# Performance work log

Hardware: AMD Instinct MI355X
Metric: run time of the kernel (lower is better)

## Reference

```python
import jax, jax.numpy as jnp
import numpy as np

S, FEAT, D, H, L, DFF, C = 1024, 64, 512, 8, 2, 2048, 10
DB = D // 4  # distance-bias MLP hidden
NFREQ = D // 6  # 85 -> 6*85=510 dims, padded to 512
EPS = 1e-5


def _layernorm(x, g, b):
    mu = jnp.mean(x, axis=-1, keepdims=True)
    var = jnp.mean(jnp.square(x - mu), axis=-1, keepdims=True)
    return (x - mu) * jax.lax.rsqrt(var + EPS) * g + b


def setup_inputs() -> dict:
    key = jax.random.key(0)
    ks = iter(jax.random.split(key, 40))
    def w(shape, scale=0.02):
        return (jax.random.normal(next(ks), shape, jnp.float32) * scale)
    inp = {
        'features': jax.random.normal(next(ks), (S, FEAT), jnp.float32),
        'positions': jax.random.uniform(next(ks), (S, 3), jnp.float32),
        'freq_bands': jnp.asarray(10.0 ** np.linspace(0.0, 10.0, NFREQ), jnp.float32),
        'in_w': w((FEAT, D)), 'in_b': jnp.zeros((D,), jnp.float32),
        'qw': w((L, D, D)), 'qb': jnp.zeros((L, D), jnp.float32),
        'kw': w((L, D, D)), 'kb': jnp.zeros((L, D), jnp.float32),
        'vw': w((L, D, D)), 'vb': jnp.zeros((L, D), jnp.float32),
        'ow': w((L, D, D)), 'ob': jnp.zeros((L, D), jnp.float32),
        'db1w': w((L, 1, DB), 0.5), 'db1b': jnp.zeros((L, DB), jnp.float32),
        'db2w': w((L, DB, H), 0.1), 'db2b': jnp.zeros((L, H), jnp.float32),
        'n1g': jnp.ones((L, D), jnp.float32), 'n1b': jnp.zeros((L, D), jnp.float32),
        'n2g': jnp.ones((L, D), jnp.float32), 'n2b': jnp.zeros((L, D), jnp.float32),
        'f1w': w((L, D, DFF)), 'f1b': jnp.zeros((L, DFF), jnp.float32),
        'f2w': w((L, DFF, D)), 'f2b': jnp.zeros((L, D), jnp.float32),
        'c1w': w((D, D // 2)), 'c1b': jnp.zeros((D // 2,), jnp.float32),
        'c2w': w((D // 2, C)), 'c2b': jnp.zeros((C,), jnp.float32),
    }
    return inp


def _forward(features, positions, freq_bands, in_w, in_b, qw, qb, kw, kb, vw, vb,
             ow, ob, db1w, db1b, db2w, db2b, n1g, n1b, n2g, n2b,
             f1w, f1b, f2w, f2b, c1w, c1b, c2w, c2b):
    d_model = in_w.shape[1]
    nhead = db2w.shape[-1]
    head_dim = d_model // nhead
    scale = 1.0 / np.sqrt(head_dim)

    x = features[None] @ in_w + in_b            # [1, S, D]
    pos = positions[None]                        # [1, S, 3]

    # 3D sinusoidal positional encoding: [sin0,cos0,sin1,cos1,sin2,cos2]
    enc = []
    for i in range(3):
        cs = pos[..., i:i + 1] * freq_bands      # [1, S, NFREQ] (broadcast)
        enc.append(jnp.sin(cs))
        enc.append(jnp.cos(cs))
    pe = jnp.concatenate(enc, axis=-1)           # [1, S, 6*NFREQ]
    if pe.shape[-1] > d_model:
        pe = pe[..., :d_model]
    elif pe.shape[-1] < d_model:
        pe = jnp.pad(pe, ((0, 0), (0, 0), (0, d_model - pe.shape[-1])))
    x = x + pe

    # pairwise distances [1, S, S, 1]; safe sqrt (zero grad on diagonal)
    diff = pos[:, :, None, :] - pos[:, None, :, :]
    sq = jnp.sum(jnp.square(diff), axis=-1, keepdims=True)
    dist = jnp.sqrt(jnp.where(sq > 0, sq, 1.0)) * (sq > 0)

    n_layers = qw.shape[0]
    seq = x.shape[1]
    for l in range(n_layers):
        q = (x @ qw[l] + qb[l]).reshape(1, seq, nhead, head_dim)
        k = (x @ kw[l] + kb[l]).reshape(1, seq, nhead, head_dim)
        v = (x @ vw[l] + vb[l]).reshape(1, seq, nhead, head_dim)
        scores = jnp.einsum('bihd,bjhd->bhij', q, k) * scale  # [1,H,S,S]
        hbias = jax.nn.relu(dist @ db1w[l] + db1b[l])          # [1,S,S,DB]
        bias = jnp.einsum('bijc,ch->bhij', hbias, db2w[l]) + db2b[l][None, :, None, None]
        attn = jax.nn.softmax(scores + bias, axis=-1)
        out = jnp.einsum('bhij,bjhd->bihd', attn, v).reshape(1, seq, d_model)
        out = out @ ow[l] + ob[l]
        x = _layernorm(x + out, n1g[l], n1b[l])
        ffn = jax.nn.relu(x @ f1w[l] + f1b[l]) @ f2w[l] + f2b[l]
        x = _layernorm(x + ffn, n2g[l], n2b[l])

    pooled = jnp.mean(x, axis=1)                 # [1, D]
    return jax.nn.relu(pooled @ c1w + c1b) @ c2w + c2b  # [1, C]


def reference(features, positions, freq_bands, in_w, in_b, qw, qb, kw, kb, vw, vb,
              ow, ob, db1w, db1b, db2w, db2b, n1g, n1b, n2g, n2b,
              f1w, f1b, f2w, f2b, c1w, c1b, c2w, c2b):
    return _forward(features, positions, freq_bands, in_w, in_b, qw, qb, kw, kb, vw, vb,
                    ow, ob, db1w, db1b, db2w, db2b, n1g, n1b, n2g, n2b,
                    f1w, f1b, f2w, f2b, c1w, c1b, c2w, c2b)
```

## Files before the change

### kernel.cpp

```cpp
#include <hip/hip_runtime.h>

namespace {
constexpr int kS   = 1024;
constexpr int kD   = 512;
constexpr int kDFF = 2048;
constexpr int kNF  = 85;
}

typedef __attribute__((ext_vector_type(8))) short bhalf8_t;
typedef _Float16 half8_t __attribute__((ext_vector_type(8)));
typedef __attribute__((ext_vector_type(4))) float f32x4_t;

__device__ __forceinline__ float wave_sum(float v) {
#pragma unroll
    for (int o = 1; o < 64; o <<= 1) v += __shfl_xor(v, o, 64);
    return v;
}
__device__ __forceinline__ unsigned short f2h(float f) {
    _Float16 h = (_Float16)f;
    return __builtin_bit_cast(unsigned short, h);
}
__device__ __forceinline__ float h2f(unsigned short u) {
    return (float)__builtin_bit_cast(_Float16, u);
}

__device__ __forceinline__ void tr_tile32(const float* __restrict__ in,
                                          unsigned short* __restrict__ out,
                                          int N, int K, int k0, int n0, int t,
                                          float* tile )
{
    int r = t >> 3, c4 = (t & 7) * 4;
    float4 v = *reinterpret_cast<const float4*>(&in[(long)(k0 + r) * N + n0 + c4]);
    tile[r * 33 + c4] = v.x; tile[r * 33 + c4 + 1] = v.y;
    tile[r * 33 + c4 + 2] = v.z; tile[r * 33 + c4 + 3] = v.w;
    __syncthreads();
    int nr = t >> 3, kq = (t & 7) * 4;
    unsigned short h[4];
#pragma unroll
    for (int j = 0; j < 4; ++j) h[j] = f2h(tile[(kq + j) * 33 + nr]);
    *reinterpret_cast<ushort4*>(&out[(long)(n0 + nr) * K + k0 + kq]) =
        make_ushort4(h[0], h[1], h[2], h[3]);
}

__global__ __launch_bounds__(256)
void prep_k(const float* __restrict__ feat, const float* __restrict__ pos,
            const float* __restrict__ fb, const float* __restrict__ in_w,
            const float* __restrict__ in_b, float* __restrict__ x,
            unsigned short* __restrict__ xb, float* __restrict__ dist,
            const float* __restrict__ qw, const float* __restrict__ kw,
            const float* __restrict__ vw, const float* __restrict__ ow,
            unsigned short* __restrict__ qwb, unsigned short* __restrict__ kwb,
            unsigned short* __restrict__ vwb, unsigned short* __restrict__ owb,
            const float* __restrict__ f1w, unsigned short* __restrict__ f1wb,
            const float* __restrict__ f2w, unsigned short* __restrict__ f2wb,
            const float* __restrict__ a_, const float* __restrict__ b_,
            const float* __restrict__ w2, const float* __restrict__ b2,
            float* __restrict__ bp_out, float* __restrict__ Atab,
            float* __restrict__ Btab)
{
    __shared__ float smem[1056];
    int bid = blockIdx.x;
    int t = threadIdx.x;
    if (bid < 256) {
        int s0 = bid * 4;
        smem[t] = feat[s0 * 64 + t];
        __syncthreads();
        float b0 = in_b[t], b1 = in_b[t + 256];
        float a0[4] = {b0, b0, b0, b0}, a1[4] = {b1, b1, b1, b1};
#pragma unroll 4
        for (int c = 0; c < 64; ++c) {
            float w0 = in_w[c * kD + t], w1 = in_w[c * kD + 256 + t];
#pragma unroll
            for (int r = 0; r < 4; ++r) {
                a0[r] = fmaf(smem[r * 64 + c], w0, a0[r]);
                a1[r] = fmaf(smem[r * 64 + c], w1, a1[r]);
            }
        }
#pragma unroll
        for (int r = 0; r < 4; ++r) {
            int s = s0 + r;
            float pe0 = 0.f, pe1 = 0.f;
            int d = t;
            if (d < 6 * kNF) {
                int seg = d / kNF, idx = d - seg * kNF;
                float cs = pos[s * 3 + (seg >> 1)] * fb[idx];
                pe0 = (seg & 1) ? cosf(cs) : sinf(cs);
            }
            d = t + 256;
            if (d < 6 * kNF) {
                int seg = d / kNF, idx = d - seg * kNF;
                float cs = pos[s * 3 + (seg >> 1)] * fb[idx];
                pe1 = (seg & 1) ? cosf(cs) : sinf(cs);
            }
            float o0 = a0[r] + pe0, o1 = a1[r] + pe1;
            x[s * kD + t]        = o0;
            x[s * kD + 256 + t]  = o1;
            xb[s * kD + t]       = f2h(o0);
            xb[s * kD + 256 + t] = f2h(o1);
        }
    } else if (bid < 1280) {
        int i = bid - 256;
        float px = pos[i * 3], py = pos[i * 3 + 1], pz = pos[i * 3 + 2];
        for (int j = t; j < kS; j += 256) {
            float dx = px - pos[j * 3], dy = py - pos[j * 3 + 1], dz = pz - pos[j * 3 + 2];
            float sq = dx * dx + dy * dy + dz * dz;
            dist[(long)i * kS + j] = sq > 0.f ? sqrtf(sq) : 0.f;
        }
    } else if (bid < 7424) {
        int idx = bid - 1280;
        if (idx < 2048) {
            int zz = idx >> 8, rem = idx & 255;
            int mat = zz >> 1, layer = zz & 1;
            const float* in = (mat == 0) ? qw : (mat == 1) ? kw : (mat == 2) ? vw : ow;
            unsigned short* out = (mat == 0) ? qwb : (mat == 1) ? kwb : (mat == 2) ? vwb : owb;
            tr_tile32(in + (long)layer * 262144, out + (long)layer * 262144,
                      512, 512, (rem & 15) * 32, (rem >> 4) * 32, t, smem);
        } else if (idx < 4096) {
            int l = idx - 2048;
            int z = l >> 10;
            tr_tile32(f1w + (long)z * 1048576, f1wb + (long)z * 1048576,
                      2048, 512, (l & 15) * 32, ((l >> 4) & 63) * 32, t, smem);
        } else {
            int l = idx - 4096;
            int z = l >> 10;
            tr_tile32(f2w + (long)z * 1048576, f2wb + (long)z * 1048576,
                      512, 2048, (l & 63) * 32, ((l >> 6) & 15) * 32, t, smem);
        }
    } else {
        int l = bid - 7424;
        int seg = l % 129, ly = l / 129;
        const float* ap = a_ + ly * 128;
        const float* bpp = b_ + ly * 128;
        const float* w2p = w2 + ly * 1024;
        const float* b2p = b2 + ly * 8;
        float* At = Atab + ly * 1040;
        float* Bt = Btab + ly * 1040;

        if (t < 128) {
            float a = ap[t], b = bpp[t];
            smem[t] = (a != 0.f) ? (-b / a) : 3.0e38f;
        }
        __syncthreads();
        for (int ksz = 2; ksz <= 128; ksz <<= 1) {
            for (int j = ksz >> 1; j > 0; j >>= 1) {
                if (t < 128) {
                    int ixj = t ^ j;
                    if (ixj > t) {
                        bool up = ((t & ksz) == 0);
                        float x0 = smem[t], x1 = smem[ixj];
                        if ((x0 > x1) == up) { smem[t] = x1; smem[ixj] = x0; }
                    }
                }
                __syncthreads();
            }
        }
        float m;
        if (seg == 0)        m = smem[0] - 1.0f;
        else if (seg == 128) m = smem[127] + 1.0f;
        else                 m = 0.5f * (smem[seg - 1] + smem[seg]);
        if (seg == 0 && t < 128) bp_out[ly * 128 + t] = smem[t];
        __syncthreads();

        int h = t & 7, cg = t >> 3;
        float A = 0.f, B = 0.f;
#pragma unroll
        for (int j = 0; j < 4; ++j) {
            int c = cg * 4 + j;
            float a = ap[c], b = bpp[c];
            if (fmaf(a, m, b) > 0.f) {
                float w = w2p[c * 8 + h];
                A = fmaf(a, w, A);
                B = fmaf(b, w, B);
            }
        }
#pragma unroll
        for (int off = 8; off < 64; off <<= 1) {
            A += __shfl_xor(A, off, 64);
            B += __shfl_xor(B, off, 64);
        }
        int w = t >> 6, lane = t & 63;
        if (lane < 8) { smem[w * 8 + lane] = A; smem[32 + w * 8 + lane] = B; }
        __syncthreads();
        if (t < 8) {
            float At_ = smem[t] + smem[8 + t] + smem[16 + t] + smem[24 + t];
            float Bt_ = smem[32 + t] + smem[40 + t] + smem[48 + t] + smem[56 + t];
            At[seg * 8 + t] = At_;
            Bt[seg * 8 + t] = Bt_ + b2p[t];
        }
    }
}

constexpr int BKp = 72;
constexpr int ASZ = 64 * BKp;
constexpr int BSZ = 128 * BKp;

template<int K>
__device__ __forceinline__ void gemm_core(
    const unsigned short* __restrict__ Ap, const unsigned short* __restrict__ Bp,
    int lda, int ldb, int bm, int bn, int tid,
    unsigned short* __restrict__ As, unsigned short* __restrict__ Bs,
    f32x4_t acc[2][4])
{
    int w = tid >> 6, lane = tid & 63, quad = lane >> 4, l16 = lane & 15;
    int wm = (w >> 1) * 32, wn = (w & 1) * 64;
    int ar = tid >> 2, ac = (tid & 3) * 16;
    int br = tid >> 1, bc = (tid & 1) * 32;
    const unsigned short* pa = Ap + (long)(bm + ar) * lda + ac;
    const unsigned short* pb = Bp + (long)(bn + br) * ldb + bc;

    bhalf8_t a0_0, a0_1, b0_0, b0_1, b0_2, b0_3;
    bhalf8_t a1_0, a1_1, b1_0, b1_1, b1_2, b1_3;

#define LDG(S, k0) do { \
    a##S##_0 = *reinterpret_cast<const bhalf8_t*>(pa + (k0)); \
    a##S##_1 = *reinterpret_cast<const bhalf8_t*>(pa + (k0) + 8); \
    b##S##_0 = *reinterpret_cast<const bhalf8_t*>(pb + (k0)); \
    b##S##_1 = *reinterpret_cast<const bhalf8_t*>(pb + (k0) + 8); \
    b##S##_2 = *reinterpret_cast<const bhalf8_t*>(pb + (k0) + 16); \
    b##S##_3 = *reinterpret_cast<const bhalf8_t*>(pb + (k0) + 24); } while (0)
#define STG(S, as, bs) do { \
    *reinterpret_cast<bhalf8_t*>(&(as)[ar * BKp + ac])      = a##S##_0; \
    *reinterpret_cast<bhalf8_t*>(&(as)[ar * BKp + ac + 8])  = a##S##_1; \
    *reinterpret_cast<bhalf8_t*>(&(bs)[br * BKp + bc])      = b##S##_0; \
    *reinterpret_cast<bhalf8_t*>(&(bs)[br * BKp + bc + 8])  = b##S##_1; \
    *reinterpret_cast<bhalf8_t*>(&(bs)[br * BKp + bc + 16]) = b##S##_2; \
    *reinterpret_cast<bhalf8_t*>(&(bs)[br * BKp + bc + 24]) = b##S##_3; } while (0)

    constexpr int NT = K / 64;
    LDG(0, 0);
    STG(0, As, Bs);
    if (NT > 1) LDG(1, 64);
#pragma unroll
    for (int t = 0; t < NT; ++t) {
        __syncthreads();
        if (t + 2 < NT) {
            if ((t & 1) == 0) LDG(0, (t + 2) * 64);
            else              LDG(1, (t + 2) * 64);
        }
        const unsigned short* as = As + (t & 1) * ASZ;
        const unsigned short* bs = Bs + (t & 1) * BSZ;
#pragma unroll
        for (int kq = 0; kq < 2; ++kq) {
            bhalf8_t af[2], bf[4];
#pragma unroll
            for (int i = 0; i < 2; ++i)
                af[i] = *reinterpret_cast<const bhalf8_t*>(
                    &as[(wm + i * 16 + l16) * BKp + kq * 32 + quad * 8]);
#pragma unroll
            for (int j = 0; j < 4; ++j)
                bf[j] = *reinterpret_cast<const bhalf8_t*>(
                    &bs[(wn + j * 16 + l16) * BKp + kq * 32 + quad * 8]);
#pragma unroll
            for (int i = 0; i < 2; ++i)
#pragma unroll
                for (int j = 0; j < 4; ++j)
                    acc[i][j] = __builtin_amdgcn_mfma_f32_16x16x32_f16(
                        __builtin_bit_cast(half8_t, af[i]), __builtin_bit_cast(half8_t, bf[j]),
                        acc[i][j], 0, 0, 0);
        }
        if (t + 1 < NT) {
            if (((t + 1) & 1) == 0) STG(0, As, Bs);
            else                    STG(1, As + ASZ, Bs + BSZ);
        }
    }
#undef LDG
#undef STG
}

__global__ __launch_bounds__(256, 2)
void qkv_bias_k(const unsigned short* __restrict__ xb,
                const unsigned short* __restrict__ qwb, const unsigned short* __restrict__ kwb,
                const unsigned short* __restrict__ vwb,
                const float* __restrict__ qbias, const float* __restrict__ kbias,
                const float* __restrict__ vbias,
                unsigned short* __restrict__ qb2, unsigned short* __restrict__ kb2,
                unsigned short* __restrict__ vtb,
                const float* __restrict__ dist, const float* __restrict__ bp,
                const float* __restrict__ Atab, const float* __restrict__ Btab,
                unsigned short* __restrict__ bmap, unsigned int* __restrict__ cnt)
{
    __shared__ __align__(16) unsigned short smem[2 * ASZ + 2 * BSZ];
    int bid = blockIdx.x;
    int tid = threadIdx.x;
    if (bid < 192) {
        int z = bid >> 6, rem = bid & 63;
        int bm = (rem & 15) * 64, bn = (rem >> 4) * 128;
        const unsigned short* Bp = (z == 1) ? kwb : (z == 2) ? vwb : qwb;
        const float* bias = (z == 1) ? kbias : (z == 2) ? vbias : qbias;
        f32x4_t acc[2][4] = {};
        gemm_core<512>(xb, Bp, 512, 512, bm, bn, tid, smem, smem + 2 * ASZ, acc);

        int w = tid >> 6, lane = tid & 63, quad = lane >> 4, l16 = lane & 15;
        int wm = (w >> 1) * 32, wn = (w & 1) * 64;
        if (z == 2) {
            __syncthreads();
            unsigned short* T = smem;
#pragma unroll
            for (int j = 0; j < 4; ++j) {
                int ln = wn + j * 16 + l16;
                float bv = bias[bn + ln];
#pragma unroll
                for (int i = 0; i < 2; ++i)
#pragma unroll
                    for (int r = 0; r < 4; ++r)
                        T[ln * BKp + wm + i * 16 + quad * 4 + r] =
                            f2h((acc[i][j][r] + bv) * 1024.f);
            }
            __syncthreads();
            int nr = tid >> 1, mc = (tid & 1) * 32;
            int gn = bn + nr;
            unsigned short* dst = vtb + (long)(gn >> 6) * 65536
                                + (long)(gn & 63) * 1024 + bm + mc;
#pragma unroll
            for (int jj = 0; jj < 4; ++jj)
                *reinterpret_cast<bhalf8_t*>(dst + jj * 8) =
                    *reinterpret_cast<const bhalf8_t*>(&T[nr * BKp + mc + jj * 8]);
        } else {
#pragma unroll
            for (int j = 0; j < 4; ++j) {
                int n = bn + wn + j * 16 + l16;
                float bv = bias[n];
                unsigned short* dst = ((z == 1) ? kb2 : qb2)
                    + (long)(n >> 6) * 131072 + (n & 63);
#pragma unroll
                for (int i = 0; i < 2; ++i)
#pragma unroll
                    for (int r = 0; r < 4; ++r) {
                        int m = bm + wm + i * 16 + quad * 4 + r;
                        float s = acc[i][j][r] + bv;
                        unsigned short hi = f2h(s);
                        dst[(long)m * 128]      = hi;
                        dst[(long)m * 128 + 64] = (z == 0) ? f2h(s - h2f(hi)) : hi;
                    }
            }
        }
    } else {
        if (bid == 192 && tid < 8) cnt[tid] = 0;
        float* fs = reinterpret_cast<float*>(smem);
        float* bps = fs;
        float* Ah  = fs + 128;
        float* Bh  = fs + 1160;
        int t = tid;
        if (t < 128) bps[t] = bp[t];
        for (int i = t; i < 1032; i += 256) { Ah[i] = Atab[i]; Bh[i] = Btab[i]; }
        __syncthreads();
        long i = ((long)(bid - 192) * 256 + t) * 4;
        float4 d4 = *reinterpret_cast<const float4*>(dist + i);
        float dv[4] = {d4.x, d4.y, d4.z, d4.w};
        int seg[4];
#pragma unroll
        for (int j = 0; j < 4; ++j) {
            float tv = dv[j];
            int lo = 0, hi = 128;
            while (lo < hi) { int mid = (lo + hi) >> 1; if (bps[mid] < tv) lo = mid + 1; else hi = mid; }
            seg[j] = lo;
        }
        long gm  = i >> 10;
        int gn0  = (int)(i & 1023);
        int zz   = gn0 >> 7, nb = (gn0 >> 4) & 7, c4 = gn0 & 15;
        long pbase = gm * 1024 + zz * 128 + nb;
#pragma unroll
        for (int h = 0; h < 8; ++h) {
            unsigned short* bh = bmap + (long)h * 1048576 + pbase;
#pragma unroll
            for (int j = 0; j < 4; ++j)
                bh[(c4 + j) * 8] =
                    f2h(fmaf(Ah[seg[j] * 8 + h], dv[j], Bh[seg[j] * 8 + h]));
        }
    }
}

__global__ __launch_bounds__(256, 2)
void bgemm_ffn1_k(const unsigned short* __restrict__ A,
                  const unsigned short* __restrict__ B,
                  const float* __restrict__ bias,
                  unsigned short* __restrict__ hb)
{
    __shared__ __align__(16) unsigned short smem[2 * ASZ + 2 * BSZ];
    int tid = threadIdx.x;
    int bm = blockIdx.x * 64, bn = blockIdx.y * 128;
    f32x4_t acc[2][4] = {};
    gemm_core<512>(A, B, 512, 512, bm, bn, tid, smem, smem + 2 * ASZ, acc);

    int w = tid >> 6, lane = tid & 63, quad = lane >> 4, l16 = lane & 15;
    int wm = (w >> 1) * 32, wn = (w & 1) * 64;
#pragma unroll
    for (int j = 0; j < 4; ++j) {
        int n = bn + wn + j * 16 + l16;
        float bv = bias[n];
#pragma unroll
        for (int i = 0; i < 2; ++i)
#pragma unroll
            for (int r = 0; r < 4; ++r) {
                int m = bm + wm + i * 16 + quad * 4 + r;
                hb[(long)m * kDFF + n] = f2h(fmaxf(acc[i][j][r] + bv, 0.f));
            }
    }
}

template<int K>
__global__ __launch_bounds__(256, 2)
void bgemm_k(const unsigned short* __restrict__ A, const unsigned short* __restrict__ B,
             int N, int lda, int ldb, unsigned short* __restrict__ Cpart)
{
    __shared__ __align__(16) unsigned short smem[2 * ASZ + 2 * BSZ];
    int tid = threadIdx.x;
    int ks = blockIdx.z;
    const unsigned short* Ap = A + (long)ks * K;
    const unsigned short* Bp = B + (long)ks * K;
    int bm = blockIdx.x * 64, bn = blockIdx.y * 128;
    f32x4_t acc[2][4] = {};
    gemm_core<K>(Ap, Bp, lda, ldb, bm, bn, tid, smem, smem + 2 * ASZ, acc);

    int w = tid >> 6, lane = tid & 63, quad = lane >> 4, l16 = lane & 15;
    int wm = (w >> 1) * 32, wn = (w & 1) * 64;
    unsigned short* Cp = Cpart + (long)ks * kS * N;
#pragma unroll
    for (int i = 0; i < 2; ++i)
#pragma unroll
        for (int j = 0; j < 4; ++j)
#pragma unroll
            for (int r = 0; r < 4; ++r) {
                int m = bm + wm + i * 16 + quad * 4 + r;
                int n = bn + wn + j * 16 + l16;
                Cp[(long)m * N + n] = f2h(acc[i][j][r]);
            }
}

__global__ __launch_bounds__(256, 2)
void bgemm_oproj_k(const unsigned short* __restrict__ po,
                   const float* __restrict__ pm, const float* __restrict__ pl,
                   const unsigned short* __restrict__ Bw,
                   unsigned short* __restrict__ Cpart)
{
    __shared__ __align__(16) unsigned short As[2 * ASZ];
    __shared__ __align__(16) unsigned short Bs[2 * BSZ];
    __shared__ float wz_s[2][64][9];
    __shared__ float inv_s[2][64];

    int tid = threadIdx.x;
    int ks = blockIdx.z;
    int bm = blockIdx.x * 64, bn = blockIdx.y * 128;
    int h0 = ks * 2;

    int br = tid >> 1, bc = (tid & 1) * 32;
    {
        const unsigned short* pb = Bw + (long)(bn + br) * 512 + ks * 128 + bc;
#pragma unroll
        for (int t = 0; t < 2; ++t) {
            bhalf8_t v0 = *reinterpret_cast<const bhalf8_t*>(pb + t * 64);
            bhalf8_t v1 = *reinterpret_cast<const bhalf8_t*>(pb + t * 64 + 8);
            bhalf8_t v2 = *reinterpret_cast<const bhalf8_t*>(pb + t * 64 + 16);
            bhalf8_t v3 = *reinterpret_cast<const bhalf8_t*>(pb + t * 64 + 24);
            unsigned short* bs = Bs + t * BSZ;
            *reinterpret_cast<bhalf8_t*>(&bs[br * BKp + bc])      = v0;
            *reinterpret_cast<bhalf8_t*>(&bs[br * BKp + bc + 8])  = v1;
            *reinterpret_cast<bhalf8_t*>(&bs[br * BKp + bc + 16]) = v2;
            *reinterpret_cast<bhalf8_t*>(&bs[br * BKp + bc + 24]) = v3;
        }
    }

    if (tid < 128) {
        int t = tid >> 6, r = tid & 63;
        long sidx = (long)(h0 + t) * 1024 + bm + r;
        float m[8], M = -3.0e38f;
#pragma unroll
        for (int z = 0; z < 8; ++z) { m[z] = pm[z * 8192 + sidx]; M = fmaxf(M, m[z]); }
        float lt = 0.f;
#pragma unroll
        for (int z = 0; z < 8; ++z) {
            float w = __expf(m[z] - M);
            wz_s[t][r][z] = w;
            lt = fmaf(pl[z * 8192 + sidx], w, lt);
        }
        inv_s[t][r] = 1.f / lt;
    }
    __syncthreads();

    int ar = tid >> 2, ac = (tid & 3) * 16;
#pragma unroll
    for (int t = 0; t < 2; ++t) {
        float inv = inv_s[t][ar];
        const unsigned short* p = po + ((long)(h0 + t) * 1024 + bm + ar) * 64 + ac;
        float acc[16] = {};
#pragma unroll
        for (int z = 0; z < 8; ++z) {
            float w = wz_s[t][ar][z];
            bhalf8_t v0 = *reinterpret_cast<const bhalf8_t*>(p + (long)z * 524288);
            bhalf8_t v1 = *reinterpret_cast<const bhalf8_t*>(p + (long)z * 524288 + 8);
#pragma unroll
            for (int j = 0; j < 8; ++j) {
                acc[j]     = fmaf(h2f((unsigned short)v0[j]), w, acc[j]);
                acc[8 + j] = fmaf(h2f((unsigned short)v1[j]), w, acc[8 + j]);
            }
        }
        unsigned short* as = As + t * ASZ;
#pragma unroll
        for (int j = 0; j < 16; ++j)
            as[ar * BKp + ac + j] = f2h(acc[j] * inv);
    }
    __syncthreads();

    int w = tid >> 6, lane = tid & 63, quad = lane >> 4, l16 = lane & 15;
    int wm = (w >> 1) * 32, wn = (w & 1) * 64;
    f32x4_t accf[2][4] = {};
#pragma unroll
    for (int t = 0; t < 2; ++t) {
        const unsigned short* as = As + t * ASZ;
        const unsigned short* bs = Bs + t * BSZ;
#pragma unroll
        for (int kq = 0; kq < 2; ++kq) {
            bhalf8_t af[2], bf[4];
#pragma unroll
            for (int i = 0; i < 2; ++i)
                af[i] = *reinterpret_cast<const bhalf8_t*>(
                    &as[(wm + i * 16 + l16) * BKp + kq * 32 + quad * 8]);
#pragma unroll
            for (int j = 0; j < 4; ++j)
                bf[j] = *reinterpret_cast<const bhalf8_t*>(
                    &bs[(wn + j * 16 + l16) * BKp + kq * 32 + quad * 8]);
#pragma unroll
            for (int i = 0; i < 2; ++i)
#pragma unroll
                for (int j = 0; j < 4; ++j)
                    accf[i][j] = __builtin_amdgcn_mfma_f32_16x16x32_f16(
                        __builtin_bit_cast(half8_t, af[i]), __builtin_bit_cast(half8_t, bf[j]),
                        accf[i][j], 0, 0, 0);
        }
    }

    unsigned short* Cp = Cpart + (long)ks * kS * 512;
#pragma unroll
    for (int i = 0; i < 2; ++i)
#pragma unroll
        for (int j = 0; j < 4; ++j)
#pragma unroll
            for (int r = 0; r < 4; ++r) {
                int m = bm + wm + i * 16 + quad * 4 + r;
                int n = bn + wn + j * 16 + l16;
                Cp[(long)m * 512 + n] = f2h(accf[i][j][r]);
            }
}

__global__ __launch_bounds__(256, 3)
void flash_part_k(const unsigned short* __restrict__ qb2, const unsigned short* __restrict__ kb2,
                  const unsigned short* __restrict__ vtb, const unsigned short* __restrict__ bmap,
                  unsigned short* __restrict__ po, float* __restrict__ pm, float* __restrict__ pl)
{
    constexpr int KP = 136;
    __shared__ __align__(16) unsigned short Klds[128 * KP];
    __shared__ __align__(16) unsigned short Vlds[64 * KP];

    int tid = threadIdx.x;
    int w    = tid >> 6;
    int lane = tid & 63;
    int quad = lane >> 4, l16 = lane & 15;

    int wg  = blockIdx.x;
    int lin = (wg & 7) * 128 + (wg >> 3);
    int qbg = lin & 15;
    int h   = (lin >> 4) & 7;
    int z   = lin >> 7;
    int qb  = qbg * 4 + w;
    int bm  = qb * 16;
    int k0  = z * 128;

    const unsigned short* Qh = qb2 + (long)h * 131072;
    const unsigned short* Kh = kb2 + (long)h * 131072;
    const unsigned short* Vh = vtb + (long)h * 65536;
    const unsigned short* Bm = bmap + (long)h * 1048576;

    {
        int kr = tid >> 1, kc = (tid & 1) * 64;
#pragma unroll
        for (int j = 0; j < 8; ++j)
            *reinterpret_cast<bhalf8_t*>(&Klds[kr * KP + kc + j * 8]) =
                *reinterpret_cast<const bhalf8_t*>(&Kh[(long)(k0 + kr) * 128 + kc + j * 8]);
        int vr = tid >> 2, vc = (tid & 3) * 32;
#pragma unroll
        for (int j = 0; j < 4; ++j)
            *reinterpret_cast<bhalf8_t*>(&Vlds[vr * KP + vc + j * 8]) =
                *reinterpret_cast<const bhalf8_t*>(&Vh[(long)vr * 1024 + k0 + vc + j * 8]);
    }

    bhalf8_t aq[4];
#pragma unroll
    for (int kq = 0; kq < 4; ++kq)
        aq[kq] = *reinterpret_cast<const bhalf8_t*>(
            &Qh[(long)(bm + l16) * 128 + kq * 32 + quad * 8]);
    bhalf8_t bias8[4];
#pragma unroll
    for (int r = 0; r < 4; ++r) {
        int gm = bm + quad * 4 + r;
        bias8[r] = *reinterpret_cast<const bhalf8_t*>(
            &Bm[(long)gm * 1024 + z * 128 + l16 * 8]);
    }

    __syncthreads();

    f32x4_t sacc[8] = {};
#pragma unroll
    for (int kq = 0; kq < 4; ++kq) {
        bhalf8_t bk[8];
#pragma unroll
        for (int nb = 0; nb < 8; ++nb)
            bk[nb] = *reinterpret_cast<const bhalf8_t*>(
                &Klds[(nb * 16 + l16) * KP + kq * 32 + quad * 8]);
#pragma unroll
        for (int nb = 0; nb < 8; ++nb)
            sacc[nb] = __builtin_amdgcn_mfma_f32_16x16x32_f16(
                __builtin_bit_cast(half8_t, aq[kq]), __builtin_bit_cast(half8_t, bk[nb]),
                sacc[nb], 0, 0, 0);
    }

    float m_r[4] = {-3.0e38f, -3.0e38f, -3.0e38f, -3.0e38f};
#pragma unroll
    for (int nb = 0; nb < 8; ++nb)
#pragma unroll
        for (int r = 0; r < 4; ++r) {
            float bias = h2f((unsigned short)bias8[r][nb]);
            float s = fmaf(sacc[nb][r], 0.125f, bias);
            sacc[nb][r] = s;
            m_r[r] = fmaxf(m_r[r], s);
        }
#pragma unroll
    for (int r = 0; r < 4; ++r) {
        float m_ = m_r[r];
#pragma unroll
        for (int off = 1; off < 16; off <<= 1) m_ = fmaxf(m_, __shfl_xor(m_, off, 64));
        m_r[r] = m_;
    }

    __syncthreads();

    unsigned short* Ps = Klds + w * 16 * KP;
    float l_r[4];
#pragma unroll
    for (int r = 0; r < 4; ++r) {
        int row = quad * 4 + r;
        float mN = m_r[r];
        float s_ = 0.f;
#pragma unroll
        for (int nb = 0; nb < 8; ++nb) {
            float p = __expf(sacc[nb][r] - mN);
            Ps[row * KP + nb * 16 + l16] = f2h(p * 16384.f);
            s_ += p;
        }
#pragma unroll
        for (int off = 1; off < 16; off <<= 1) s_ += __shfl_xor(s_, off, 64);
        l_r[r] = s_;
    }

    long sbase = (((long)z * 8 + h) * 64 + qb) * 16;
    if (l16 == 0) {
#pragma unroll
        for (int r = 0; r < 4; ++r) {
            pm[sbase + quad * 4 + r] = m_r[r];
            pl[sbase + quad * 4 + r] = l_r[r];
        }
    }

    f32x4_t oacc[4] = {};
#pragma unroll
    for (int kq2 = 0; kq2 < 4; ++kq2) {
        bhalf8_t ap = *reinterpret_cast<const bhalf8_t*>(&Ps[l16 * KP + kq2 * 32 + quad * 8]);
#pragma unroll
        for (int j2 = 0; j2 < 4; ++j2) {
            bhalf8_t bv = *reinterpret_cast<const bhalf8_t*>(
                &Vlds[(j2 * 16 + l16) * KP + kq2 * 32 + quad * 8]);
            oacc[j2] = __builtin_amdgcn_mfma_f32_16x16x32_f16(
                __builtin_bit_cast(half8_t, ap), __builtin_bit_cast(half8_t, bv),
                oacc[j2], 0, 0, 0);
        }
    }

    unsigned short* pob = po + sbase * 64;
#pragma unroll
    for (int j2 = 0; j2 < 4; ++j2)
#pragma unroll
        for (int r = 0; r < 4; ++r)
            pob[(quad * 4 + r) * 64 + j2 * 16 + l16] =
                f2h(oacc[j2][r] * (1.f / 16777216.f));
}

__global__ __launch_bounds__(256)
void add_ln_fused_k(const unsigned short* __restrict__ part, float* __restrict__ x,
                    const float* __restrict__ bias,
                    const float* __restrict__ g, const float* __restrict__ b,
                    unsigned short* __restrict__ xb, int splitk)
{
    __shared__ float sm[4];
    int row = blockIdx.x, t = threadIdx.x;
    const long MN = (long)kS * kD;
    float* xr = x + (long)row * kD;
    float s0 = 0.f, s1 = 0.f;
    const unsigned short* pr = part + (long)row * kD;
    for (int sl = 0; sl < splitk; ++sl) {
        s0 += h2f(pr[(long)sl * MN + t]);
        s1 += h2f(pr[(long)sl * MN + t + 256]);
    }
    s0 += bias[t] + xr[t];
    s1 += bias[t + 256] + xr[t + 256];
    float sum = wave_sum(s0 + s1);
    if ((t & 63) == 0) sm[t >> 6] = sum;
    __syncthreads();
    sum = sm[0] + sm[1] + sm[2] + sm[3];
    float mu = sum * (1.f / kD);
    float d0 = s0 - mu, d1 = s1 - mu;
    __syncthreads();
    float vs = wave_sum(d0 * d0 + d1 * d1);
    if ((t & 63) == 0) sm[t >> 6] = vs;
    __syncthreads();
    vs = sm[0] + sm[1] + sm[2] + sm[3];
    float rs = rsqrtf(vs * (1.f / kD) + 1e-5f);
    float o0 = fmaf(d0 * rs, g[t], b[t]);
    float o1 = fmaf(d1 * rs, g[t + 256], b[t + 256]);
    xr[t]       = o0;
    xr[t + 256] = o1;
    unsigned short* xrow = xb + (long)row * 512;
    xrow[t]       = f2h(o0);
    xrow[t + 256] = f2h(o1);
}

__global__ __launch_bounds__(256)
void pool_head_k(const float* __restrict__ x, float* __restrict__ partial,
                 float* __restrict__ h1g, unsigned int* __restrict__ cnt2,
                 const float* __restrict__ c1w, const float* __restrict__ c1b,
                 const float* __restrict__ c2w, const float* __restrict__ c2b,
                 float* __restrict__ out)
{
    __shared__ float pooled[kD];
    __shared__ int flag;
    int t = threadIdx.x;
    int bid = blockIdx.x;
    int cb = bid & 1, rb = bid >> 1;
    int col = cb * 256 + t;
    float s = 0.f;
    for (int r = rb * 128; r < rb * 128 + 128; ++r) s += x[(long)r * kD + col];
    partial[rb * kD + col] = s;

    __threadfence();
    if (t == 0) {
        atomicAdd(&cnt2[0], 1u);
        while (atomicAdd(&cnt2[0], 0u) < 16u) {}
    }
    __syncthreads();
    __threadfence();

    {
        float p0 = 0.f, p1 = 0.f;
#pragma unroll
        for (int r = 0; r < 8; ++r) {
            p0 += partial[r * kD + t];
            p1 += partial[r * kD + t + 256];
        }
        pooled[t]       = p0 * (1.0f / kS);
        pooled[t + 256] = p1 * (1.0f / kS);
    }
    __syncthreads();

    {
        int c = bid * 16 + (t >> 4);
        int sub = t & 15;
        float a = 0.f;
        for (int f = sub; f < kD; f += 16)
            a = fmaf(pooled[f], c1w[(long)f * 256 + c], a);
#pragma unroll
        for (int o = 1; o < 16; o <<= 1) a += __shfl_xor(a, o, 64);
        if (sub == 0) h1g[c] = fmaxf(a + c1b[c], 0.f);
    }

    __threadfence();
    if (t == 0) flag = (atomicAdd(&cnt2[1], 1u) == 15u);
    __syncthreads();
    if (!flag) return;
    __threadfence();

    if (t < 160) {
        int c = t >> 4, sub = t & 15;
        float a = 0.f;
        for (int f = sub; f < 256; f += 16)
            a = fmaf(h1g[f], c2w[(long)f * 10 + c], a);
#pragma unroll
        for (int o = 1; o < 16; o <<= 1) a += __shfl_xor(a, o, 64);
        if (sub == 0) out[c] = a + c2b[c];
    }
}

extern "C" void kernel_launch(void* const* d_in, const int* in_sizes, int n_in,
                              void* d_out, int out_size, void* d_ws, size_t ws_size,
                              hipStream_t stream)
{
    (void)in_sizes; (void)n_in; (void)out_size; (void)ws_size;
    const float* features = (const float*)d_in[0];
    const float* positions= (const float*)d_in[1];
    const float* fb       = (const float*)d_in[2];
    const float* in_w     = (const float*)d_in[3];
    const float* in_b     = (const float*)d_in[4];
    const float* qw  = (const float*)d_in[5];
    const float* qb  = (const float*)d_in[6];
    const float* kw  = (const float*)d_in[7];
    const float* kb  = (const float*)d_in[8];
    const float* vw  = (const float*)d_in[9];
    const float* vb  = (const float*)d_in[10];
    const float* ow  = (const float*)d_in[11];
    const float* ob  = (const float*)d_in[12];
    const float* db1w= (const float*)d_in[13];
    const float* db1b= (const float*)d_in[14];
    const float* db2w= (const float*)d_in[15];
    const float* db2b= (const float*)d_in[16];
    const float* n1g = (const float*)d_in[17];
    const float* n1b = (const float*)d_in[18];
    const float* n2g = (const float*)d_in[19];
    const float* n2b = (const float*)d_in[20];
    const float* f1w = (const float*)d_in[21];
    const float* f1b = (const float*)d_in[22];
    const float* f2w = (const float*)d_in[23];
    const float* f2b = (const float*)d_in[24];
    const float* c1w = (const float*)d_in[25];
    const float* c1b = (const float*)d_in[26];
    const float* c2w = (const float*)d_in[27];
    const float* c2b = (const float*)d_in[28];

    float* ws = (float*)d_ws;
    const long SD = (long)kS * kD;
    float* x      = ws;
    float* dist   = ws + 3 * SD;
    float* part_f = ws + 5 * SD;
    float* bpw    = ws + 17 * SD;
    float* Atab   = bpw + 256;
    float* Btab   = Atab + 2080;
    float* partial= Btab + 2080;

    unsigned short* part16 = (unsigned short*)part_f;
    unsigned short* po     = (unsigned short*)part_f;
    float* pmv = part_f + 2162688;
    float* plv = pmv + 65536;
    unsigned int* cnt2 = (unsigned int*)(plv + 65536);
    float* h1g = (float*)(cnt2 + 16);
    unsigned short* part16b = (unsigned short*)(part_f + 2294048);

    unsigned short* ub = (unsigned short*)(ws + 17 * SD + 8512);
    unsigned short* xb   = ub;
    unsigned short* qb2  = ub   + 1048576;
    unsigned short* kb2  = qb2  + 1048576;
    unsigned short* vtb  = kb2  + 1048576;
    unsigned short* hb   = vtb  + 524288;
    unsigned short* qwb  = hb   + 2097152;
    unsigned short* kwb  = qwb  + 524288;
    unsigned short* vwb  = kwb  + 524288;
    unsigned short* owb  = vwb  + 524288;
    unsigned short* f1wb = owb  + 524288;
    unsigned short* f2wb = f1wb + 2097152;
    unsigned short* bmap = f2wb + 2097152;

    prep_k<<<7682, 256, 0, stream>>>(features, positions, fb, in_w, in_b, x, xb,
                                     dist, qw, kw, vw, ow, qwb, kwb, vwb, owb,
                                     f1w, f1wb, f2w, f2wb,
                                     db1w, db1b, db2w, db2b, bpw, Atab, Btab);

    for (int l = 0; l < 2; ++l) {
        qkv_bias_k<<<1216, 256, 0, stream>>>(
            xb, qwb + l * 262144, kwb + l * 262144, vwb + l * 262144,
            qb + l * kD, kb + l * kD, vb + l * kD, qb2, kb2, vtb,
            dist, bpw + l * 128, Atab + l * 1040, Btab + l * 1040, bmap, cnt2);

        flash_part_k<<<1024, 256, 0, stream>>>(
            qb2, kb2, vtb, bmap, po, pmv, plv);

        bgemm_oproj_k<<<dim3(16, 4, 4), 256, 0, stream>>>(
            po, pmv, plv, owb + l * 262144, part16b);
        add_ln_fused_k<<<kS, 256, 0, stream>>>(
            part16b, x, ob + l * kD, n1g + l * kD, n1b + l * kD, xb, 4);

        bgemm_ffn1_k<<<dim3(16, 16), 256, 0, stream>>>(
            xb, f1wb + l * 1048576, f1b + l * kDFF, hb);

        bgemm_k<512><<<dim3(16, 4, 4), 256, 0, stream>>>(
            hb, f2wb + l * 1048576, 512, 2048, 2048, part16);
        add_ln_fused_k<<<kS, 256, 0, stream>>>(
            part16, x, f2b + l * kD, n2g + l * kD, n2b + l * kD, xb, 4);
    }

    pool_head_k<<<16, 256, 0, stream>>>(x, partial, h1g, cnt2,
                                        c1w, c1b, c2w, c2b, (float*)d_out);
}
```

Before: 283.5 us.

## Stage GEMM tiles with direct global-to-LDS loads and XOR-swizzled layout

Rewrites the shared GEMM core so tiles are copied straight from global memory into LDS with global_load_lds, instead of being loaded into registers and then stored to LDS. The padded 72-element row stride is replaced by an unpadded 64-wide layout with an XOR swizzle, to avoid LDS bank conflicts on the MFMA fragment reads. The prefetch depth drops from two register stages to a single LDS double buffer. This aims to save VGPRs and LDS store instructions, at the cost of depending on correct waitcnt handling for the asynchronous LDS writes before each barrier.

```diff
diff --git a/kernel.cpp b/kernel.cpp
--- a/kernel.cpp
+++ b/kernel.cpp
@@ -190,9 +190,18 @@
     }
 }
 
+constexpr int ASZ2 = 64 * 64;
+constexpr int BSZ2 = 128 * 64;
+
 constexpr int BKp = 72;
 constexpr int ASZ = 64 * BKp;
 constexpr int BSZ = 128 * BKp;
+
+__device__ __forceinline__ void gload16(const unsigned short* g, unsigned short* l) {
+    __builtin_amdgcn_global_load_lds(
+        (const __attribute__((address_space(1))) unsigned int*)g,
+        (__attribute__((address_space(3))) unsigned int*)l, 16, 0, 0);
+}
 
 template<int K>
 __device__ __forceinline__ void gemm_core(
@@ -203,53 +212,44 @@
 {
     int w = tid >> 6, lane = tid & 63, quad = lane >> 4, l16 = lane & 15;
     int wm = (w >> 1) * 32, wn = (w & 1) * 64;
-    int ar = tid >> 2, ac = (tid & 3) * 16;
-    int br = tid >> 1, bc = (tid & 1) * 32;
-    const unsigned short* pa = Ap + (long)(bm + ar) * lda + ac;
-    const unsigned short* pb = Bp + (long)(bn + br) * ldb + bc;
-
-    bhalf8_t a0_0, a0_1, b0_0, b0_1, b0_2, b0_3;
-    bhalf8_t a1_0, a1_1, b1_0, b1_1, b1_2, b1_3;
-
-#define LDG(S, k0) do { \
-    a##S##_0 = *reinterpret_cast<const bhalf8_t*>(pa + (k0)); \
-    a##S##_1 = *reinterpret_cast<const bhalf8_t*>(pa + (k0) + 8); \
-    b##S##_0 = *reinterpret_cast<const bhalf8_t*>(pb + (k0)); \
-    b##S##_1 = *reinterpret_cast<const bhalf8_t*>(pb + (k0) + 8); \
-    b##S##_2 = *reinterpret_cast<const bhalf8_t*>(pb + (k0) + 16); \
-    b##S##_3 = *reinterpret_cast<const bhalf8_t*>(pb + (k0) + 24); } while (0)
-#define STG(S, as, bs) do { \
-    *reinterpret_cast<bhalf8_t*>(&(as)[ar * BKp + ac])      = a##S##_0; \
-    *reinterpret_cast<bhalf8_t*>(&(as)[ar * BKp + ac + 8])  = a##S##_1; \
-    *reinterpret_cast<bhalf8_t*>(&(bs)[br * BKp + bc])      = b##S##_0; \
-    *reinterpret_cast<bhalf8_t*>(&(bs)[br * BKp + bc + 8])  = b##S##_1; \
-    *reinterpret_cast<bhalf8_t*>(&(bs)[br * BKp + bc + 16]) = b##S##_2; \
-    *reinterpret_cast<bhalf8_t*>(&(bs)[br * BKp + bc + 24]) = b##S##_3; } while (0)
+    int lr = lane >> 3;
+    int sw = (lane & 7) ^ lr;
+
+    const unsigned short* pa  = Ap + (long)(bm + w * 16 + lr) * lda + sw * 8;
+    const unsigned short* pa2 = pa + (long)8 * lda;
+    const unsigned short* pb  = Bp + (long)(bn + w * 32 + lr) * ldb + sw * 8;
+
+    auto stage = [&](int k0, int buf) {
+        unsigned short* as = As + buf * ASZ2 + w * 16 * 64;
+        unsigned short* bs = Bs + buf * BSZ2 + w * 32 * 64;
+        gload16(pa + k0, as);
+        gload16(pa2 + k0, as + 8 * 64);
+#pragma unroll
+        for (int j = 0; j < 4; ++j)
+            gload16(pb + (long)(j * 8) * ldb + k0, bs + j * 8 * 64);
+    };
 
     constexpr int NT = K / 64;
-    LDG(0, 0);
-    STG(0, As, Bs);
-    if (NT > 1) LDG(1, 64);
+    stage(0, 0);
+    int r7 = l16 & 7;
 #pragma unroll
     for (int t = 0; t < NT; ++t) {
         __syncthreads();
-        if (t + 2 < NT) {
-            if ((t & 1) == 0) LDG(0, (t + 2) * 64);
-            else              LDG(1, (t + 2) * 64);
-        }
-        const unsigned short* as = As + (t & 1) * ASZ;
-        const unsigned short* bs = Bs + (t & 1) * BSZ;
+        if (t + 1 < NT) stage((t + 1) * 64, (t + 1) & 1);
+        const unsigned short* as = As + (t & 1) * ASZ2;
+        const unsigned short* bs = Bs + (t & 1) * BSZ2;
 #pragma unroll
         for (int kq = 0; kq < 2; ++kq) {
+            int slot = ((kq * 4 + quad) ^ r7) * 8;
             bhalf8_t af[2], bf[4];
 #pragma unroll
             for (int i = 0; i < 2; ++i)
                 af[i] = *reinterpret_cast<const bhalf8_t*>(
-                    &as[(wm + i * 16 + l16) * BKp + kq * 32 + quad * 8]);
+                    &as[(wm + i * 16 + l16) * 64 + slot]);
 #pragma unroll
             for (int j = 0; j < 4; ++j)
                 bf[j] = *reinterpret_cast<const bhalf8_t*>(
-                    &bs[(wn + j * 16 + l16) * BKp + kq * 32 + quad * 8]);
+                    &bs[(wn + j * 16 + l16) * 64 + slot]);
 #pragma unroll
             for (int i = 0; i < 2; ++i)
 #pragma unroll
@@ -258,13 +258,7 @@
                         __builtin_bit_cast(half8_t, af[i]), __builtin_bit_cast(half8_t, bf[j]),
                         acc[i][j], 0, 0, 0);
         }
-        if (t + 1 < NT) {
-            if (((t + 1) & 1) == 0) STG(0, As, Bs);
-            else                    STG(1, As + ASZ, Bs + BSZ);
-        }
-    }
-#undef LDG
-#undef STG
+    }
 }
 
 __global__ __launch_bounds__(256, 2)
@@ -279,7 +273,7 @@
                 const float* __restrict__ Atab, const float* __restrict__ Btab,
                 unsigned short* __restrict__ bmap, unsigned int* __restrict__ cnt)
 {
-    __shared__ __align__(16) unsigned short smem[2 * ASZ + 2 * BSZ];
+    __shared__ __align__(16) unsigned short smem[2 * ASZ2 + 2 * BSZ2];
     int bid = blockIdx.x;
     int tid = threadIdx.x;
     if (bid < 192) {
@@ -288,7 +282,7 @@
         const unsigned short* Bp = (z == 1) ? kwb : (z == 2) ? vwb : qwb;
         const float* bias = (z == 1) ? kbias : (z == 2) ? vbias : qbias;
         f32x4_t acc[2][4] = {};
-        gemm_core<512>(xb, Bp, 512, 512, bm, bn, tid, smem, smem + 2 * ASZ, acc);
+        gemm_core<512>(xb, Bp, 512, 512, bm, bn, tid, smem, smem + 2 * ASZ2, acc);
 
         int w = tid >> 6, lane = tid & 63, quad = lane >> 4, l16 = lane & 15;
         int wm = (w >> 1) * 32, wn = (w & 1) * 64;
@@ -376,11 +370,11 @@
                   const float* __restrict__ bias,
                   unsigned short* __restrict__ hb)
 {
-    __shared__ __align__(16) unsigned short smem[2 * ASZ + 2 * BSZ];
+    __shared__ __align__(16) unsigned short smem[2 * ASZ2 + 2 * BSZ2];
     int tid = threadIdx.x;
     int bm = blockIdx.x * 64, bn = blockIdx.y * 128;
     f32x4_t acc[2][4] = {};
-    gemm_core<512>(A, B, 512, 512, bm, bn, tid, smem, smem + 2 * ASZ, acc);
+    gemm_core<512>(A, B, 512, 512, bm, bn, tid, smem, smem + 2 * ASZ2, acc);
 
     int w = tid >> 6, lane = tid & 63, quad = lane >> 4, l16 = lane & 15;
     int wm = (w >> 1) * 32, wn = (w & 1) * 64;
@@ -403,14 +397,14 @@
 void bgemm_k(const unsigned short* __restrict__ A, const unsigned short* __restrict__ B,
              int N, int lda, int ldb, unsigned short* __restrict__ Cpart)
 {
-    __shared__ __align__(16) unsigned short smem[2 * ASZ + 2 * BSZ];
+    __shared__ __align__(16) unsigned short smem[2 * ASZ2 + 2 * BSZ2];
     int tid = threadIdx.x;
     int ks = blockIdx.z;
     const unsigned short* Ap = A + (long)ks * K;
     const unsigned short* Bp = B + (long)ks * K;
     int bm = blockIdx.x * 64, bn = blockIdx.y * 128;
     f32x4_t acc[2][4] = {};
-    gemm_core<K>(Ap, Bp, lda, ldb, bm, bn, tid, smem, smem + 2 * ASZ, acc);
+    gemm_core<K>(Ap, Bp, lda, ldb, bm, bn, tid, smem, smem + 2 * ASZ2, acc);
 
     int w = tid >> 6, lane = tid & 63, quad = lane >> 4, l16 = lane & 15;
     int wm = (w >> 1) * 32, wn = (w & 1) * 64;
```

After: 284.2 us. No clear change (+0.2%).
